# Optimization experiments

Measured on AMD Instinct MI355X. Metric: run time of the kernel, lower is better.

## Reference

```python
import jax, jax.numpy as jnp
import numpy as np

B, S, M = 32, 16384, 64
IN_DIM, OUT_DIM, HID = 64, 64, 512
N_READ, N_WRITE = 1, 1
LSTM_IN = IN_DIM + OUT_DIM + M * N_READ
EPS = 1e-8  # torch F.cosine_similarity eps


def setup_inputs():
    key = jax.random.key(0)
    ks = jax.random.split(key, 16)
    w = lambda k, sh: (0.02 * jax.random.normal(k, sh)).astype(jnp.float32)
    return {
        'x_input': jax.random.normal(ks[0], (B, 1, IN_DIM), dtype=jnp.float32),
        'prev_desired_output': jax.random.normal(ks[1], (B, 1, OUT_DIM), dtype=jnp.float32),
        'prev_read_vec': jax.random.normal(ks[2], (B, 1, M * N_READ), dtype=jnp.float32),
        'memory': jax.random.normal(ks[3], (B, S, M), dtype=jnp.float32),
        'W_ih': w(ks[4], (4 * HID, LSTM_IN)),
        'W_hh': w(ks[5], (4 * HID, HID)),
        'b_ih': jnp.zeros((4 * HID,), jnp.float32),
        'b_hh': jnp.zeros((4 * HID,), jnp.float32),
        'W_r': w(ks[6], (N_READ * (M + 6), HID)),
        'b_r': jnp.zeros((N_READ * (M + 6),), jnp.float32),
        'W_w': w(ks[7], (N_WRITE * (3 * M + 6), HID)),
        'b_w': jnp.zeros((N_WRITE * (3 * M + 6),), jnp.float32),
        'W_o': w(ks[8], (OUT_DIM, HID + M * N_READ)),
        'b_o': jnp.zeros((OUT_DIM,), jnp.float32),
    }


def _addressing(h, W, b, mem, nbr_heads, is_read):
    # ctrl2head linear -> [B, H, gate_dim], then slice k/beta/g/s/gamma(/erase/add)
    out = (h @ W.T + b).reshape(h.shape[0], nbr_heads, -1)
    k = out[..., :M]
    beta = jax.nn.softplus(out[..., M:M + 1])
    g = jax.nn.sigmoid(out[..., M + 1:M + 2])
    s = jax.nn.softmax(jax.nn.softplus(out[..., M + 2:M + 5]), axis=-1)  # 3-tap shift kernel
    gamma = 1.0 + jax.nn.softplus(out[..., M + 5:M + 6])
    # content addressing: cosine similarity of key vs each slot
    dot = jnp.einsum('bhm,bsm->bhs', k, mem)
    kn = jnp.maximum(jnp.linalg.norm(k, axis=-1), EPS)   # [B,H]
    mn = jnp.maximum(jnp.linalg.norm(mem, axis=-1), EPS)  # [B,S]
    cos = dot / (kn[:, :, None] * mn[:, None, :])
    wc = jax.nn.softmax(beta * cos, axis=-1)
    # location addressing; prev_w is zeros after reset so wg = g*wc + (1-g)*0
    wg = g * wc
    # circular 3-tap shift (conv1d over circularly padded weights)
    ws = s[..., 0:1] * jnp.roll(wg, 1, axis=-1) + s[..., 1:2] * wg + s[..., 2:3] * jnp.roll(wg, -1, axis=-1)
    wgam = ws ** gamma  # sharpening
    w_final = wgam / jnp.sum(wgam, axis=-1, keepdims=True)
    if is_read:
        return w_final
    return w_final, out[..., M + 6:2 * M + 6], out[..., 2 * M + 6:3 * M + 6]


def reference(x_input, prev_desired_output, prev_read_vec, memory,
              W_ih, W_hh, b_ih, b_hh, W_r, b_r, W_w, b_w, W_o, b_o):
    # single-layer LSTM step from zero (h0, c0) = (0, 0)
    xt = jnp.concatenate([x_input, prev_desired_output, prev_read_vec], axis=2)[:, 0]
    z = xt @ W_ih.T + b_ih + b_hh  # h0 @ W_hh.T == 0
    i, f, gg, o = jnp.split(z, 4, axis=-1)
    c = jax.nn.sigmoid(i) * jnp.tanh(gg)  # c0 == 0
    h = jax.nn.sigmoid(o) * jnp.tanh(c)   # [B, HID]
    # read heads (read pre-write memory)
    w_read = _addressing(h, W_r, b_r, memory, N_READ, True)
    r = jnp.einsum('bhs,bsm->bhm', w_read, memory)  # [B, N_READ, M]
    # write heads: source per-head loop overwrites nmemory[bidx] each head,
    # so only the LAST write head takes effect -> use head -1
    w_write, erase, add = _addressing(h, W_w, b_w, memory, N_WRITE, False)
    wl, el, al = w_write[:, -1], erase[:, -1], add[:, -1]
    new_mem = memory * (1.0 - wl[:, :, None] * el[:, None, :]) + wl[:, :, None] * al[:, None, :]
    # external output: softmax(Linear(cat(h, read)))
    ext_in = jnp.concatenate([h, r.reshape(r.shape[0], -1)], axis=-1)
    output = jax.nn.softmax(ext_in @ W_o.T + b_o, axis=-1)
    return output, new_mem
```

## Files before the change

### kernel.cpp

```cpp
#include <hip/hip_runtime.h>
#include <hip/hip_bf16.h>
#include <math.h>

#define BB 32
#define SS 16384
#define MM 64
#define HID 512
#define EPSV 1e-8f

#define OFF_H    0
#define OFF_P    16384
#define OFF_SGRP 32768
#define OFF_SGWP (OFF_SGRP + BB*64)
#define OFF_RP   (OFF_SGWP + BB*64)
#define OFF_WGR  (OFF_RP + BB*64*64)
#define OFF_WGW  (OFF_WGR + BB*SS)

__device__ __forceinline__ float sigmoidf_(float x) { return 1.f / (1.f + expf(-x)); }
__device__ __forceinline__ float softplusf_(float x) {
    return (x > 0.f) ? x + log1pf(expf(-x)) : log1pf(expf(x));
}

__global__ void k_lstm(const float* __restrict__ x, const float* __restrict__ pdo,
                       const float* __restrict__ prv,
                       const float* __restrict__ W_ih, const float* __restrict__ b_ih,
                       const float* __restrict__ b_hh, float* __restrict__ ws) {
    int wid = blockIdx.x * 4 + (threadIdx.x >> 6);
    int lane = threadIdx.x & 63;
    int b = wid >> 9, t = wid & 511;
    float x0 = x[b * 64 + lane];
    float x1 = pdo[b * 64 + lane];
    float x2 = prv[b * 64 + lane];
    const float* wi = W_ih + (size_t)t * 192;
    const float* wg = W_ih + (size_t)(1024 + t) * 192;
    const float* wo = W_ih + (size_t)(1536 + t) * 192;
    float zi = x0 * wi[lane] + x1 * wi[64 + lane] + x2 * wi[128 + lane];
    float zg = x0 * wg[lane] + x1 * wg[64 + lane] + x2 * wg[128 + lane];
    float zo = x0 * wo[lane] + x1 * wo[64 + lane] + x2 * wo[128 + lane];
    #pragma unroll
    for (int off = 32; off >= 1; off >>= 1) {
        zi += __shfl_xor(zi, off);
        zg += __shfl_xor(zg, off);
        zo += __shfl_xor(zo, off);
    }
    if (lane == 0) {
        zi += b_ih[t] + b_hh[t];
        zg += b_ih[1024 + t] + b_hh[1024 + t];
        zo += b_ih[1536 + t] + b_hh[1536 + t];
        float c = sigmoidf_(zi) * tanhf(zg);
        ws[OFF_H + (size_t)b * 512 + t] = sigmoidf_(zo) * tanhf(c);
    }
}

__global__ void k_heads(const float* __restrict__ W_r, const float* __restrict__ b_r,
                        const float* __restrict__ W_w, const float* __restrict__ b_w,
                        float* __restrict__ ws) {
    int wid = blockIdx.x * 4 + (threadIdx.x >> 6);
    int lane = threadIdx.x & 63;
    int b = wid / 268, j = wid % 268;
    const float* h = ws + OFF_H + (size_t)b * 512;
    const float* wrow;
    float bias;
    if (j < 70) { wrow = W_r + (size_t)j * 512; bias = b_r[j]; }
    else        { wrow = W_w + (size_t)(j - 70) * 512; bias = b_w[j - 70]; }
    float acc = 0.f;
    #pragma unroll
    for (int c = 0; c < 8; c++) acc = fmaf(h[c * 64 + lane], wrow[c * 64 + lane], acc);
    #pragma unroll
    for (int off = 32; off >= 1; off >>= 1) acc += __shfl_xor(acc, off);
    if (lane != 0) return;
    acc += bias;
    float* P = ws + OFF_P + (size_t)b * 512;
    if (j < 70) {
        if (j < 64)       P[j] = acc;
        else if (j == 64) P[64] = softplusf_(acc);
        else if (j == 65) P[65] = sigmoidf_(acc);
        else if (j <= 68) P[96 + (j - 66)] = acc;
        else              P[69] = 1.f + softplusf_(acc);
    } else {
        int jj = j - 70;
        if (jj < 64)       P[128 + jj] = acc;
        else if (jj == 64) P[192] = softplusf_(acc);
        else if (jj == 65) P[193] = sigmoidf_(acc);
        else if (jj <= 68) P[224 + (jj - 66)] = acc;
        else if (jj == 69) P[197] = 1.f + softplusf_(acc);
        else if (jj < 134) P[256 + (jj - 70)] = acc;
        else               P[320 + (jj - 134)] = acc;
    }
}

__global__ void __launch_bounds__(256, 4)
k_scorewgam(const float* __restrict__ mem, float* __restrict__ ws) {
    int b = blockIdx.x >> 6;
    int chunk = blockIdx.x & 63;
    int tid = threadIdx.x;
    const float* P = ws + OFF_P + (size_t)b * 512;

    __shared__ float sh_kr[64], sh_kw[64];
    __shared__ float sh_er[258], sh_ew[258];
    __shared__ float par[8];
    __shared__ float lr[4], lw[4];

    if (tid < 64) {
        float kr = P[tid], kw = P[128 + tid];
        sh_kr[tid] = kr; sh_kw[tid] = kw;
        float nr = kr * kr, nw = kw * kw;
        #pragma unroll
        for (int off = 32; off >= 1; off >>= 1) {
            nr += __shfl_xor(nr, off);
            nw += __shfl_xor(nw, off);
        }
        if (tid == 0) {
            par[0] = 1.f / fmaxf(sqrtf(nr), EPSV);
            par[1] = 1.f / fmaxf(sqrtf(nw), EPSV);
            float s0 = softplusf_(P[96]), s1 = softplusf_(P[97]), s2 = softplusf_(P[98]);
            float mx = fmaxf(s0, fmaxf(s1, s2));
            float e0 = expf(s0 - mx), e1 = expf(s1 - mx), e2 = expf(s2 - mx);
            float si = 1.f / (e0 + e1 + e2);
            par[2] = e0 * si; par[3] = e1 * si; par[4] = e2 * si;
            s0 = softplusf_(P[224]); s1 = softplusf_(P[225]); s2 = softplusf_(P[226]);
            mx = fmaxf(s0, fmaxf(s1, s2));
            e0 = expf(s0 - mx); e1 = expf(s1 - mx); e2 = expf(s2 - mx);
            si = 1.f / (e0 + e1 + e2);
            par[5] = e0 * si; par[6] = e1 * si; par[7] = e2 * si;
        }
    }
    float beta_r = P[64], beta_w = P[192];
    float gamma_r = P[69], gamma_w = P[197];
    __syncthreads();
    float ikr = par[0], ikw = par[1];
    int row0 = chunk * 256;

    if (tid < 32) {
        int grp = tid >> 4, c = tid & 15;
        int hrow = grp ? ((row0 + 256) & (SS - 1)) : ((row0 - 1) & (SS - 1));
        float4 m4 = *(const float4*)(mem + ((size_t)b * SS + hrow) * 64 + c * 4);
        float4 kr4 = *(const float4*)(sh_kr + c * 4);
        float4 kw4 = *(const float4*)(sh_kw + c * 4);
        float dr = m4.x * kr4.x + m4.y * kr4.y + m4.z * kr4.z + m4.w * kr4.w;
        float dw = m4.x * kw4.x + m4.y * kw4.y + m4.z * kw4.z + m4.w * kw4.w;
        float n2 = m4.x * m4.x + m4.y * m4.y + m4.z * m4.z + m4.w * m4.w;
        #pragma unroll
        for (int off = 8; off >= 1; off >>= 1) {
            dr += __shfl_xor(dr, off);
            dw += __shfl_xor(dw, off);
            n2 += __shfl_xor(n2, off);
        }
        if (c == 0) {
            float imn = 1.f / fmaxf(sqrtf(n2), EPSV);
            int slot = grp ? 257 : 0;
            sh_er[slot] = exp2f(1.44269504f * beta_r * (dr * ikr * imn - 1.f));
            sh_ew[slot] = exp2f(1.44269504f * beta_w * (dw * ikw * imn - 1.f));
        }
    }

    int rowslot = tid >> 4, col = tid & 15;
    float4 kr4 = *(const float4*)(sh_kr + col * 4);
    float4 kw4 = *(const float4*)(sh_kw + col * 4);
    const float4* base = (const float4*)(mem + ((size_t)b * SS + row0) * 64) + tid;

    #pragma unroll
    for (int it = 0; it < 16; it += 4) {
        float4 v0 = base[(it + 0) * 256];
        float4 v1 = base[(it + 1) * 256];
        float4 v2 = base[(it + 2) * 256];
        float4 v3 = base[(it + 3) * 256];
        #pragma unroll
        for (int u = 0; u < 4; ++u) {
            float4 v = (u == 0) ? v0 : (u == 1) ? v1 : (u == 2) ? v2 : v3;
            float dr = v.x * kr4.x + v.y * kr4.y + v.z * kr4.z + v.w * kr4.w;
            float dw = v.x * kw4.x + v.y * kw4.y + v.z * kw4.z + v.w * kw4.w;
            float n2 = v.x * v.x + v.y * v.y + v.z * v.z + v.w * v.w;
            #pragma unroll
            for (int off = 8; off >= 1; off >>= 1) {
                dr += __shfl_xor(dr, off);
                dw += __shfl_xor(dw, off);
                n2 += __shfl_xor(n2, off);
            }
            if (col == 0) {
                float imn = 1.f / fmaxf(sqrtf(n2), EPSV);
                int r = (it + u) * 16 + rowslot;
                sh_er[1 + r] = exp2f(1.44269504f * beta_r * (dr * ikr * imn - 1.f));
                sh_ew[1 + r] = exp2f(1.44269504f * beta_w * (dw * ikw * imn - 1.f));
            }
        }
    }
    __syncthreads();

    float cvr = par[2] * sh_er[tid] + par[3] * sh_er[tid + 1] + par[4] * sh_er[tid + 2];
    float cvw = par[5] * sh_ew[tid] + par[6] * sh_ew[tid + 1] + par[7] * sh_ew[tid + 2];
    float wgr = exp2f(gamma_r * log2f(cvr));
    float wgw = exp2f(gamma_w * log2f(cvw));
    ws[OFF_WGR + (size_t)b * SS + row0 + tid] = wgr;
    ws[OFF_WGW + (size_t)b * SS + row0 + tid] = wgw;

    int w = tid >> 6, lane = tid & 63;
    float rr = wgr, rw2 = wgw;
    #pragma unroll
    for (int off = 32; off >= 1; off >>= 1) {
        rr += __shfl_xor(rr, off);
        rw2 += __shfl_xor(rw2, off);
    }
    if (lane == 0) { lr[w] = rr; lw[w] = rw2; }
    __syncthreads();
    if (tid == 0) {
        ws[OFF_SGRP + b * 64 + chunk] = lr[0] + lr[1] + lr[2] + lr[3];
        ws[OFF_SGWP + b * 64 + chunk] = lw[0] + lw[1] + lw[2] + lw[3];
    }
}

__global__ void k_update(const float* __restrict__ mem, float* __restrict__ ws,
                         float* __restrict__ out) {
    int b = blockIdx.x >> 6, chunk = blockIdx.x & 63, tid = threadIdx.x;
    int rowslot = tid >> 4, col = tid & 15;
    const float* P = ws + OFF_P + (size_t)b * 512;
    float4 er4 = *(const float4*)(P + 256 + col * 4);
    float4 ad4 = *(const float4*)(P + 320 + col * 4);

    __shared__ float sinv[2];
    if (tid < 64) {
        float v = ws[OFF_SGRP + b * 64 + tid];
        #pragma unroll
        for (int off = 32; off >= 1; off >>= 1) v += __shfl_xor(v, off);
        if (tid == 0) sinv[0] = 1.f / v;
    } else if (tid < 128) {
        float v = ws[OFF_SGWP + b * 64 + (tid - 64)];
        #pragma unroll
        for (int off = 32; off >= 1; off >>= 1) v += __shfl_xor(v, off);
        if (tid == 64) sinv[1] = 1.f / v;
    }
    __syncthreads();
    float isr = sinv[0], isw = sinv[1];

    const float* wgr = ws + OFF_WGR + (size_t)b * SS;
    const float* wgw = ws + OFF_WGW + (size_t)b * SS;
    float* nm = out + 2048 + (size_t)b * SS * 64;
    float4 racc = {0.f, 0.f, 0.f, 0.f};
    int row0 = chunk * 256;
    for (int it = 0; it < 16; ++it) {
        int row = row0 + it * 16 + rowslot;
        float wr = wgr[row] * isr;
        float ww = wgw[row] * isw;
        float4 v = *(const float4*)(mem + ((size_t)b * SS + row) * 64 + col * 4);
        racc.x = fmaf(wr, v.x, racc.x);
        racc.y = fmaf(wr, v.y, racc.y);
        racc.z = fmaf(wr, v.z, racc.z);
        racc.w = fmaf(wr, v.w, racc.w);
        float4 o4;
        o4.x = v.x * (1.f - ww * er4.x) + ww * ad4.x;
        o4.y = v.y * (1.f - ww * er4.y) + ww * ad4.y;
        o4.z = v.z * (1.f - ww * er4.z) + ww * ad4.z;
        o4.w = v.w * (1.f - ww * er4.w) + ww * ad4.w;
        *(float4*)(nm + (size_t)row * 64 + col * 4) = o4;
    }
    __shared__ float4 red[256];
    red[tid] = racc;
    __syncthreads();
    if (tid < 16) {
        float4 a = red[tid];
        for (int rs = 1; rs < 16; ++rs) {
            float4 t2 = red[rs * 16 + tid];
            a.x += t2.x; a.y += t2.y; a.z += t2.z; a.w += t2.w;
        }
        float* rp = ws + OFF_RP + ((size_t)b * 64 + chunk) * 64;
        rp[tid * 4 + 0] = a.x;
        rp[tid * 4 + 1] = a.y;
        rp[tid * 4 + 2] = a.z;
        rp[tid * 4 + 3] = a.w;
    }
}

__global__ void k_out(const float* __restrict__ ws, const float* __restrict__ W_o,
                      const float* __restrict__ b_o, float* __restrict__ out) {
    int b = blockIdx.x, o = threadIdx.x;
    __shared__ float sh_r[64];
    float accr = 0.f;
    for (int c = 0; c < 64; ++c) accr += ws[OFF_RP + ((size_t)b * 64 + c) * 64 + o];
    sh_r[o] = accr;
    __syncthreads();
    const float* h = ws + OFF_H + (size_t)b * 512;
    const float* w = W_o + (size_t)o * 576;
    float acc = b_o[o];
    for (int t = 0; t < 512; t++) acc = fmaf(h[t], w[t], acc);
    for (int m = 0; m < 64; m++) acc = fmaf(sh_r[m], w[512 + m], acc);
    float mx = acc;
    #pragma unroll
    for (int off = 32; off >= 1; off >>= 1) mx = fmaxf(mx, __shfl_xor(mx, off));
    float e = expf(acc - mx);
    float sm = e;
    #pragma unroll
    for (int off = 32; off >= 1; off >>= 1) sm += __shfl_xor(sm, off);
    out[b * 64 + o] = e / sm;
}

extern "C" void kernel_launch(void* const* d_in, const int* in_sizes, int n_in,
                              void* d_out, int out_size, void* d_ws, size_t ws_size,
                              hipStream_t stream) {
    const float* x    = (const float*)d_in[0];
    const float* pdo  = (const float*)d_in[1];
    const float* prv  = (const float*)d_in[2];
    const float* mem  = (const float*)d_in[3];
    const float* W_ih = (const float*)d_in[4];
    const float* b_ih = (const float*)d_in[6];
    const float* b_hh = (const float*)d_in[7];
    const float* W_r  = (const float*)d_in[8];
    const float* b_r  = (const float*)d_in[9];
    const float* W_w  = (const float*)d_in[10];
    const float* b_w  = (const float*)d_in[11];
    const float* W_o  = (const float*)d_in[12];
    const float* b_o  = (const float*)d_in[13];
    float* out = (float*)d_out;
    float* ws  = (float*)d_ws;

    k_lstm<<<BB * 512 / 4, 256, 0, stream>>>(x, pdo, prv, W_ih, b_ih, b_hh, ws);
    k_heads<<<(BB * 268) / 4, 256, 0, stream>>>(W_r, b_r, W_w, b_w, ws);
    k_scorewgam<<<BB * 64, 256, 0, stream>>>(mem, ws);
    k_update<<<BB * 64, 256, 0, stream>>>(mem, ws, out);
    k_out<<<BB, 64, 0, stream>>>(ws, W_o, b_o, out);
}
```

Measured before the change: 100.7 us.

## Stage memory tile in swizzled LDS and compute row scores per thread

```diff
diff --git a/kernel.cpp b/kernel.cpp
--- a/kernel.cpp
+++ b/kernel.cpp
@@ -11,8 +11,8 @@
 #define OFF_H    0
 #define OFF_P    16384
 #define OFF_SGRP 32768
-#define OFF_SGWP (OFF_SGRP + BB*64)
-#define OFF_RP   (OFF_SGWP + BB*64)
+#define OFF_SGWP (OFF_SGRP + BB*128)
+#define OFF_RP   (OFF_SGWP + BB*128)
 #define OFF_WGR  (OFF_RP + BB*64*64)
 #define OFF_WGW  (OFF_WGR + BB*SS)
 
@@ -89,21 +89,26 @@
     }
 }
 
-__global__ void __launch_bounds__(256, 4)
+__global__ void __launch_bounds__(128, 2)
 k_scorewgam(const float* __restrict__ mem, float* __restrict__ ws) {
-    int b = blockIdx.x >> 6;
-    int chunk = blockIdx.x & 63;
+    int b = blockIdx.x >> 7;
+    int chunk = blockIdx.x & 127;
     int tid = threadIdx.x;
     const float* P = ws + OFF_P + (size_t)b * 512;
-
-    __shared__ float sh_kr[64], sh_kw[64];
-    __shared__ float sh_er[258], sh_ew[258];
+    int row0 = chunk * 128;
+
+    __shared__ float4 tile[128 * 16];
+    __shared__ float sh_er[130], sh_ew[130];
     __shared__ float par[8];
-    __shared__ float lr[4], lw[4];
+    __shared__ float lr[2], lw[2];
+
+    const float4* src = (const float4*)(mem + ((size_t)b * SS + row0) * 64);
+    float4 st[16];
+    #pragma unroll
+    for (int j = 0; j < 16; ++j) st[j] = src[tid + j * 128];
 
     if (tid < 64) {
         float kr = P[tid], kw = P[128 + tid];
-        sh_kr[tid] = kr; sh_kw[tid] = kw;
         float nr = kr * kr, nw = kw * kw;
         #pragma unroll
         for (int off = 32; off >= 1; off >>= 1) {
@@ -127,16 +132,13 @@
     }
     float beta_r = P[64], beta_w = P[192];
     float gamma_r = P[69], gamma_w = P[197];
-    __syncthreads();
-    float ikr = par[0], ikw = par[1];
-    int row0 = chunk * 256;
 
     if (tid < 32) {
         int grp = tid >> 4, c = tid & 15;
-        int hrow = grp ? ((row0 + 256) & (SS - 1)) : ((row0 - 1) & (SS - 1));
+        int hrow = grp ? ((row0 + 128) & (SS - 1)) : ((row0 - 1) & (SS - 1));
         float4 m4 = *(const float4*)(mem + ((size_t)b * SS + hrow) * 64 + c * 4);
-        float4 kr4 = *(const float4*)(sh_kr + c * 4);
-        float4 kw4 = *(const float4*)(sh_kw + c * 4);
+        float4 kr4 = *(const float4*)(P + c * 4);
+        float4 kw4 = *(const float4*)(P + 128 + c * 4);
         float dr = m4.x * kr4.x + m4.y * kr4.y + m4.z * kr4.z + m4.w * kr4.w;
         float dw = m4.x * kw4.x + m4.y * kw4.y + m4.z * kw4.z + m4.w * kw4.w;
         float n2 = m4.x * m4.x + m4.y * m4.y + m4.z * m4.z + m4.w * m4.w;
@@ -148,42 +150,38 @@
         }
         if (c == 0) {
             float imn = 1.f / fmaxf(sqrtf(n2), EPSV);
-            int slot = grp ? 257 : 0;
-            sh_er[slot] = exp2f(1.44269504f * beta_r * (dr * ikr * imn - 1.f));
-            sh_ew[slot] = exp2f(1.44269504f * beta_w * (dw * ikw * imn - 1.f));
-        }
-    }
-
-    int rowslot = tid >> 4, col = tid & 15;
-    float4 kr4 = *(const float4*)(sh_kr + col * 4);
-    float4 kw4 = *(const float4*)(sh_kw + col * 4);
-    const float4* base = (const float4*)(mem + ((size_t)b * SS + row0) * 64) + tid;
-
-    #pragma unroll
-    for (int it = 0; it < 16; it += 4) {
-        float4 v0 = base[(it + 0) * 256];
-        float4 v1 = base[(it + 1) * 256];
-        float4 v2 = base[(it + 2) * 256];
-        float4 v3 = base[(it + 3) * 256];
-        #pragma unroll
-        for (int u = 0; u < 4; ++u) {
-            float4 v = (u == 0) ? v0 : (u == 1) ? v1 : (u == 2) ? v2 : v3;
-            float dr = v.x * kr4.x + v.y * kr4.y + v.z * kr4.z + v.w * kr4.w;
-            float dw = v.x * kw4.x + v.y * kw4.y + v.z * kw4.z + v.w * kw4.w;
-            float n2 = v.x * v.x + v.y * v.y + v.z * v.z + v.w * v.w;
-            #pragma unroll
-            for (int off = 8; off >= 1; off >>= 1) {
-                dr += __shfl_xor(dr, off);
-                dw += __shfl_xor(dw, off);
-                n2 += __shfl_xor(n2, off);
-            }
-            if (col == 0) {
-                float imn = 1.f / fmaxf(sqrtf(n2), EPSV);
-                int r = (it + u) * 16 + rowslot;
-                sh_er[1 + r] = exp2f(1.44269504f * beta_r * (dr * ikr * imn - 1.f));
-                sh_ew[1 + r] = exp2f(1.44269504f * beta_w * (dw * ikw * imn - 1.f));
-            }
-        }
+            int slot = grp ? 129 : 0;
+            sh_er[slot] = exp2f(1.44269504f * beta_r * (dr * par[0] * imn - 1.f));
+            sh_ew[slot] = exp2f(1.44269504f * beta_w * (dw * par[1] * imn - 1.f));
+        }
+    }
+
+    #pragma unroll
+    for (int j = 0; j < 16; ++j) {
+        int idx = tid + j * 128;
+        int r = idx >> 4, c4 = idx & 15;
+        tile[r * 16 + (c4 ^ (r & 15))] = st[j];
+    }
+    __syncthreads();
+    float ikr = par[0], ikw = par[1];
+
+    {
+        int r = tid, rx = tid & 15;
+        const float4* Pk = (const float4*)P;
+        const float4* Pw = (const float4*)(P + 128);
+        float dr = 0.f, dw = 0.f, n2 = 0.f;
+        #pragma unroll
+        for (int k = 0; k < 16; ++k) {
+            float4 m4 = tile[r * 16 + (k ^ rx)];
+            float4 kr4 = Pk[k];
+            float4 kw4 = Pw[k];
+            dr = fmaf(m4.x, kr4.x, fmaf(m4.y, kr4.y, fmaf(m4.z, kr4.z, fmaf(m4.w, kr4.w, dr))));
+            dw = fmaf(m4.x, kw4.x, fmaf(m4.y, kw4.y, fmaf(m4.z, kw4.z, fmaf(m4.w, kw4.w, dw))));
+            n2 = fmaf(m4.x, m4.x, fmaf(m4.y, m4.y, fmaf(m4.z, m4.z, fmaf(m4.w, m4.w, n2))));
+        }
+        float imn = 1.f / fmaxf(sqrtf(n2), EPSV);
+        sh_er[1 + r] = exp2f(1.44269504f * beta_r * (dr * ikr * imn - 1.f));
+        sh_ew[1 + r] = exp2f(1.44269504f * beta_w * (dw * ikw * imn - 1.f));
     }
     __syncthreads();
 
@@ -204,8 +202,8 @@
     if (lane == 0) { lr[w] = rr; lw[w] = rw2; }
     __syncthreads();
     if (tid == 0) {
-        ws[OFF_SGRP + b * 64 + chunk] = lr[0] + lr[1] + lr[2] + lr[3];
-        ws[OFF_SGWP + b * 64 + chunk] = lw[0] + lw[1] + lw[2] + lw[3];
+        ws[OFF_SGRP + b * 128 + chunk] = lr[0] + lr[1];
+        ws[OFF_SGWP + b * 128 + chunk] = lw[0] + lw[1];
     }
 }
 
@@ -219,12 +217,13 @@
 
     __shared__ float sinv[2];
     if (tid < 64) {
-        float v = ws[OFF_SGRP + b * 64 + tid];
+        float v = ws[OFF_SGRP + b * 128 + tid] + ws[OFF_SGRP + b * 128 + 64 + tid];
         #pragma unroll
         for (int off = 32; off >= 1; off >>= 1) v += __shfl_xor(v, off);
         if (tid == 0) sinv[0] = 1.f / v;
     } else if (tid < 128) {
-        float v = ws[OFF_SGWP + b * 64 + (tid - 64)];
+        int t2 = tid - 64;
+        float v = ws[OFF_SGWP + b * 128 + t2] + ws[OFF_SGWP + b * 128 + 64 + t2];
         #pragma unroll
         for (int off = 32; off >= 1; off >>= 1) v += __shfl_xor(v, off);
         if (tid == 64) sinv[1] = 1.f / v;
@@ -314,7 +313,7 @@
 
     k_lstm<<<BB * 512 / 4, 256, 0, stream>>>(x, pdo, prv, W_ih, b_ih, b_hh, ws);
     k_heads<<<(BB * 268) / 4, 256, 0, stream>>>(W_r, b_r, W_w, b_w, ws);
-    k_scorewgam<<<BB * 64, 256, 0, stream>>>(mem, ws);
+    k_scorewgam<<<BB * 128, 128, 0, stream>>>(mem, ws);
     k_update<<<BB * 64, 256, 0, stream>>>(mem, ws, out);
     k_out<<<BB, 64, 0, stream>>>(ws, W_o, b_o, out);
 }
```

Result: slower. 105.0 us (+4.3%).
